# Kernel optimization log

Measured on AMD Instinct MI355X. Metric: run time of the kernel, lower is better.

Reference implementation:

```python
import jax, jax.numpy as jnp
import numpy as np

N = 100000      # nodes
D = 128         # input feature dim
K = 8           # propagation hops (concat K+1 blocks)
HID = 512
OUT = 32
E = 1600000     # edges (avg degree 16)
BN_EPS = 1e-5
DEG_EPS = 1e-8


def setup_inputs() -> dict:
    key = jax.random.key(0)
    ks = jax.random.split(key, 8)
    feature = jax.random.normal(ks[0], (N, D), dtype=jnp.float32)
    coor = jax.random.uniform(ks[1], (N, 2), dtype=jnp.float32)
    edge_index = jax.random.randint(ks[2], (2, E), 0, N, dtype=jnp.int32)
    theta = jnp.array(1.0, dtype=jnp.float32)  # Gaussian bandwidth param
    fan1 = D * (K + 1)
    W1 = jax.random.normal(ks[3], (HID, fan1), dtype=jnp.float32) * (1.0 / np.sqrt(fan1))
    b1 = jnp.zeros((HID,), dtype=jnp.float32)
    gamma = jnp.ones((HID,), dtype=jnp.float32)
    beta = jnp.zeros((HID,), dtype=jnp.float32)
    W2 = jax.random.normal(ks[4], (OUT, HID), dtype=jnp.float32) * (1.0 / np.sqrt(HID))
    b2 = jnp.zeros((OUT,), dtype=jnp.float32)
    return {"feature": feature, "coor": coor, "theta": theta,
            "W1": W1, "b1": b1, "gamma": gamma, "beta": beta,
            "W2": W2, "b2": b2, "edge_index": edge_index, "m": 1}


def reference(feature, coor, theta, W1, b1, gamma, beta, W2, b2, edge_index, m):
    row, col = edge_index[0], edge_index[1]  # dst, src
    # Gaussian kernel edge weights from coordinate distances (gather on coor)
    diff = coor[row] - coor[col]                       # [E, 2]
    dist2 = jnp.sum(diff * diff, axis=-1)              # [E]
    w = jnp.exp(-dist2 * theta / m)                    # [E]
    # degree (row) normalization via scatter-add
    deg = jax.ops.segment_sum(w, row, num_segments=N)  # [N]
    norm = w / (deg[row] + DEG_EPS)                    # [E]
    # K sequential propagations, concat with input (-> N x D*(K+1))
    xs = [feature]
    x = feature
    for _ in range(K):
        msgs = x[col] * norm[:, None]                  # [E, D] gather + weight
        x = jax.ops.segment_sum(msgs, row, num_segments=N)  # [N, D] scatter
        xs.append(x)
    h = jnp.concatenate(xs, axis=-1)                   # [N, D*(K+1)]
    # MLP head: fc1 -> leaky_relu(0.2) -> BatchNorm1d (batch stats) -> fc2
    h = jax.nn.leaky_relu(h @ W1.T + b1, negative_slope=0.2)
    mu = jnp.mean(h, axis=0)
    var = jnp.var(h, axis=0)
    h = (h - mu) * jax.lax.rsqrt(var + BN_EPS) * gamma + beta
    # dropout omitted (deterministic/eval reference)
    return h @ W2.T + b2
```

## Files before the change

### kernel.cpp

```cpp
#include <hip/hip_runtime.h>
#include <hip/hip_bf16.h>
#include <cstdint>
#include <cstddef>

#define NNODES 100000
#define DFEAT 128
#define KHOP 8
#define FAN1 1152
#define HIDN 512
#define OUTD 32
#define NEDGE 1600000
#define BN_EPS 1e-5f
#define DEG_EPS 1e-8f

using short8 = __attribute__((ext_vector_type(8))) short;
using f32x4  = __attribute__((ext_vector_type(4))) float;

__device__ __forceinline__ float bf16lo(uint32_t u) { return __uint_as_float(u << 16); }
__device__ __forceinline__ float bf16hi(uint32_t u) { return __uint_as_float(u & 0xffff0000u); }
__device__ __forceinline__ float bf16s(short x) {
    return __uint_as_float(((uint32_t)(uint16_t)x) << 16);
}
__device__ __forceinline__ uint32_t packbf(float a, float b) {
    uint32_t lo = __bfloat16_as_ushort(__float2bfloat16(a));
    uint32_t hi = __bfloat16_as_ushort(__float2bfloat16(b));
    return lo | (hi << 16);
}

__device__ __forceinline__ void gload16(const void* g, void* l) {
    __builtin_amdgcn_global_load_lds(
        (const __attribute__((address_space(1))) uint32_t*)g,
        (__attribute__((address_space(3))) uint32_t*)l, 16, 0, 0);
}

struct Blk9 { const __hip_bfloat16* p[9]; };

__global__ __launch_bounds__(256) void edge_kernel(
    const int* __restrict__ ei, const float* __restrict__ coor,
    const float* __restrict__ theta, const int* __restrict__ mm,
    float* __restrict__ deg, int* __restrict__ cnt)
{
    int e = blockIdx.x * 256 + threadIdx.x;
    if (e >= NEDGE) return;
    float tom = theta[0] / (float)mm[0];
    int r = ei[e], c = ei[NEDGE + e];
    float2 pr = *(const float2*)(coor + 2*(size_t)r);
    float2 pc = *(const float2*)(coor + 2*(size_t)c);
    float dx = pr.x - pc.x, dy = pr.y - pc.y;
    float w = expf(-(dx*dx + dy*dy) * tom);
    atomicAdd(&deg[r], w);
    atomicAdd(&cnt[r], 1);
}

__global__ __launch_bounds__(1024) void scan_local(
    const int* __restrict__ cnt, int* __restrict__ row_ptr,
    int* __restrict__ bsum, int n)
{
    __shared__ int wsum[16];
    int b = blockIdx.x, tid = threadIdx.x;
    int i = b * 1024 + tid;
    int lane = tid & 63, wv = tid >> 6;
    int v = (i < n) ? cnt[i] : 0;
    #pragma unroll
    for (int off = 1; off < 64; off <<= 1) {
        int t = __shfl_up(v, off, 64);
        if (lane >= off) v += t;
    }
    if (lane == 63) wsum[wv] = v;
    __syncthreads();
    if (tid < 16) {
        int t = wsum[tid];
        #pragma unroll
        for (int off = 1; off < 16; off <<= 1) {
            int u = __shfl_up(t, off, 64);
            if (tid >= off) t += u;
        }
        wsum[tid] = t;
    }
    __syncthreads();
    int incl = v + ((wv == 0) ? 0 : wsum[wv - 1]);
    if (i < n) row_ptr[i + 1] = incl;
    if (tid == 0) bsum[b] = wsum[15];
}

__global__ __launch_bounds__(128) void scan_carry(int* __restrict__ bsum, int n)
{
    __shared__ int ws[2];
    int tid = threadIdx.x, lane = tid & 63, wv = tid >> 6;
    int v = (tid < n) ? bsum[tid] : 0;
    int incl = v;
    #pragma unroll
    for (int off = 1; off < 64; off <<= 1) {
        int t = __shfl_up(incl, off, 64);
        if (lane >= off) incl += t;
    }
    if (lane == 63) ws[wv] = incl;
    __syncthreads();
    int excl = incl - v + ((wv == 0) ? 0 : ws[0]);
    if (tid < n) bsum[tid] = excl;
}

__global__ __launch_bounds__(256) void scan_add(
    const int* __restrict__ bsum, int* __restrict__ row_ptr, int n)
{
    int i = blockIdx.x * 256 + threadIdx.x;
    if (i == 0) row_ptr[0] = 0;
    if (i < n) row_ptr[i + 1] += bsum[i >> 10];
}

__global__ __launch_bounds__(256) void fill_kernel(
    const int* __restrict__ ei, const float* __restrict__ coor,
    const float* __restrict__ theta, const int* __restrict__ mm,
    const float* __restrict__ deg, const int* __restrict__ row_ptr,
    int* __restrict__ fill, int* __restrict__ cols, float* __restrict__ nrm)
{
    int e = blockIdx.x * 256 + threadIdx.x;
    if (e >= NEDGE) return;
    float tom = theta[0] / (float)mm[0];
    int r = ei[e], c = ei[NEDGE + e];
    float2 pr = *(const float2*)(coor + 2*(size_t)r);
    float2 pc = *(const float2*)(coor + 2*(size_t)c);
    float dx = pr.x - pc.x, dy = pr.y - pc.y;
    float w = expf(-(dx*dx + dy*dy) * tom);
    int pos = row_ptr[r] + atomicAdd(&fill[r], 1);
    cols[pos] = c;
    nrm[pos] = w / (deg[r] + DEG_EPS);
}

__global__ __launch_bounds__(256) void cast_feat_kernel(
    const float* __restrict__ f, __hip_bfloat16* __restrict__ x0)
{
    int i = blockIdx.x * 256 + threadIdx.x;
    int node = i >> 6, l2 = i & 63;
    if (node >= NNODES) return;
    float2 v = *(const float2*)(f + (size_t)node * DFEAT + l2 * 2);
    __hip_bfloat162 hb;
    hb.x = __float2bfloat16(v.x);
    hb.y = __float2bfloat16(v.y);
    *(__hip_bfloat162*)(x0 + (size_t)node * DFEAT + l2 * 2) = hb;
}

__global__ __launch_bounds__(256) void cast_w1_kernel(
    const float* __restrict__ w1, __hip_bfloat16* __restrict__ o)
{
    int i = blockIdx.x * 256 + threadIdx.x;
    if (i < HIDN * FAN1) o[i] = __float2bfloat16(w1[i]);
}

__global__ __launch_bounds__(256) void prop_kernel(
    const __hip_bfloat16* __restrict__ x, __hip_bfloat16* __restrict__ y,
    const int* __restrict__ row_ptr, const int* __restrict__ cols,
    const float* __restrict__ nrm)
{
    int gw = (blockIdx.x * 256 + threadIdx.x) >> 6;
    if (gw >= NNODES) return;
    int lane = threadIdx.x & 63;
    int q = lane >> 4, sl = lane & 15;
    int beg = row_ptr[gw], end = row_ptr[gw + 1];
    float a0 = 0.f, a1 = 0.f, a2 = 0.f, a3 = 0.f;
    float a4 = 0.f, a5 = 0.f, a6 = 0.f, a7 = 0.f;
    int e = beg + q;
    for (; e + 12 < end; e += 16) {
        int s0 = cols[e], s1 = cols[e + 4], s2 = cols[e + 8], s3 = cols[e + 12];
        float w0 = nrm[e], w1 = nrm[e + 4], w2 = nrm[e + 8], w3 = nrm[e + 12];
        uint4 u0 = *(const uint4*)(x + (size_t)s0 * DFEAT + sl * 8);
        uint4 u1 = *(const uint4*)(x + (size_t)s1 * DFEAT + sl * 8);
        uint4 u2 = *(const uint4*)(x + (size_t)s2 * DFEAT + sl * 8);
        uint4 u3 = *(const uint4*)(x + (size_t)s3 * DFEAT + sl * 8);
        a0 += w0 * bf16lo(u0.x); a1 += w0 * bf16hi(u0.x);
        a2 += w0 * bf16lo(u0.y); a3 += w0 * bf16hi(u0.y);
        a4 += w0 * bf16lo(u0.z); a5 += w0 * bf16hi(u0.z);
        a6 += w0 * bf16lo(u0.w); a7 += w0 * bf16hi(u0.w);
        a0 += w1 * bf16lo(u1.x); a1 += w1 * bf16hi(u1.x);
        a2 += w1 * bf16lo(u1.y); a3 += w1 * bf16hi(u1.y);
        a4 += w1 * bf16lo(u1.z); a5 += w1 * bf16hi(u1.z);
        a6 += w1 * bf16lo(u1.w); a7 += w1 * bf16hi(u1.w);
        a0 += w2 * bf16lo(u2.x); a1 += w2 * bf16hi(u2.x);
        a2 += w2 * bf16lo(u2.y); a3 += w2 * bf16hi(u2.y);
        a4 += w2 * bf16lo(u2.z); a5 += w2 * bf16hi(u2.z);
        a6 += w2 * bf16lo(u2.w); a7 += w2 * bf16hi(u2.w);
        a0 += w3 * bf16lo(u3.x); a1 += w3 * bf16hi(u3.x);
        a2 += w3 * bf16lo(u3.y); a3 += w3 * bf16hi(u3.y);
        a4 += w3 * bf16lo(u3.z); a5 += w3 * bf16hi(u3.z);
        a6 += w3 * bf16lo(u3.w); a7 += w3 * bf16hi(u3.w);
    }
    for (; e < end; e += 4) {
        int s0 = cols[e];
        float w0 = nrm[e];
        uint4 u0 = *(const uint4*)(x + (size_t)s0 * DFEAT + sl * 8);
        a0 += w0 * bf16lo(u0.x); a1 += w0 * bf16hi(u0.x);
        a2 += w0 * bf16lo(u0.y); a3 += w0 * bf16hi(u0.y);
        a4 += w0 * bf16lo(u0.z); a5 += w0 * bf16hi(u0.z);
        a6 += w0 * bf16lo(u0.w); a7 += w0 * bf16hi(u0.w);
    }
    a0 += __shfl_xor(a0, 16, 64); a0 += __shfl_xor(a0, 32, 64);
    a1 += __shfl_xor(a1, 16, 64); a1 += __shfl_xor(a1, 32, 64);
    a2 += __shfl_xor(a2, 16, 64); a2 += __shfl_xor(a2, 32, 64);
    a3 += __shfl_xor(a3, 16, 64); a3 += __shfl_xor(a3, 32, 64);
    a4 += __shfl_xor(a4, 16, 64); a4 += __shfl_xor(a4, 32, 64);
    a5 += __shfl_xor(a5, 16, 64); a5 += __shfl_xor(a5, 32, 64);
    a6 += __shfl_xor(a6, 16, 64); a6 += __shfl_xor(a6, 32, 64);
    a7 += __shfl_xor(a7, 16, 64); a7 += __shfl_xor(a7, 32, 64);
    if (q == 0) {
        uint4 o;
        o.x = packbf(a0, a1);
        o.y = packbf(a2, a3);
        o.z = packbf(a4, a5);
        o.w = packbf(a6, a7);
        *(uint4*)(y + (size_t)gw * DFEAT + sl * 8) = o;
    }
}

__global__ __launch_bounds__(256) void fc1_kernel(
    Blk9 blks, const __hip_bfloat16* __restrict__ w1,
    const float* __restrict__ b1, __hip_bfloat16* __restrict__ h1,
    float* __restrict__ gsum, float* __restrict__ gsq,
    int nblk, int kb0, int mode)
{
    __shared__ char smem[33792];
    int pid = blockIdx.x;
    int lid = (pid & 7) * 391 + (pid >> 3);
    int n0 = (lid & 3) * 128;
    int m0 = (lid >> 2) * 128;
    int tid = threadIdx.x, lane = tid & 63, wv = tid >> 6;
    int wr = wv >> 1, wc = wv & 1;

    f32x4 acc[4][4];
    #pragma unroll
    for (int i = 0; i < 4; ++i)
        #pragma unroll
        for (int j = 0; j < 4; ++j)
            acc[i][j] = (f32x4){0.f, 0.f, 0.f, 0.f};

    int nkt = nblk * 4;

#define STAGE(hb, ktv) do {                                                   \
        const __hip_bfloat16* xp = blks.p[(ktv) >> 2];                        \
        int koff_ = ((ktv) & 3) * 32;                                         \
        int kglob_ = (kb0 + ((ktv) >> 2)) * 128 + koff_;                      \
        char* Ab_ = smem + (hb) * 16384;                                      \
        char* Bb_ = Ab_ + 8192;                                               \
        _Pragma("unroll")                                                     \
        for (int l = 0; l < 2; ++l) {                                         \
            int u = l * 256 + wv * 64 + lane;                                 \
            int row_ = u >> 2, qq_ = u & 3;                                   \
            gload16(xp + (size_t)(m0 + row_) * DFEAT + koff_ + qq_ * 8,       \
                    Ab_ + u * 16);                                            \
            gload16(w1 + (size_t)(n0 + row_) * FAN1 + kglob_ + qq_ * 8,       \
                    Bb_ + u * 16);                                            \
        }                                                                     \
    } while (0)

    STAGE(0, 0);
    for (int kt = 0; kt < nkt; ++kt) {
        int cur = kt & 1;
        __builtin_amdgcn_s_barrier();
        if (kt + 1 < nkt) {
            STAGE(cur ^ 1, kt + 1);
            asm volatile("s_waitcnt vmcnt(4)" ::: "memory");
        } else {
            asm volatile("s_waitcnt vmcnt(0)" ::: "memory");
        }
        __builtin_amdgcn_s_barrier();
        char* Ab = smem + cur * 16384;
        char* Bb = Ab + 8192;
        short8 af[4], bfr[4];
        #pragma unroll
        for (int i = 0; i < 4; ++i)
            af[i] = *(const short8*)(Ab + (wr * 64 + i * 16 + (lane & 15)) * 64 + (lane >> 4) * 16);
        #pragma unroll
        for (int j = 0; j < 4; ++j)
            bfr[j] = *(const short8*)(Bb + (wc * 64 + j * 16 + (lane & 15)) * 64 + (lane >> 4) * 16);
        #pragma unroll
        for (int j = 0; j < 4; ++j)
            #pragma unroll
            for (int i = 0; i < 4; ++i)
                acc[i][j] = __builtin_amdgcn_mfma_f32_16x16x32_bf16(af[i], bfr[j], acc[i][j], 0, 0, 0);
    }
#undef STAGE

    __syncthreads();
    __hip_bfloat16* tile = (__hip_bfloat16*)smem;
    float* lsum = (float*)(smem + 32768);
    float* lsq  = lsum + 128;
    bool fin = (mode & 2) != 0;
    if (fin && tid < 128) { lsum[tid] = 0.f; lsq[tid] = 0.f; }
    #pragma unroll
    for (int i = 0; i < 4; ++i) {
        #pragma unroll
        for (int j = 0; j < 4; ++j) {
            int col = wc * 64 + j * 16 + (lane & 15);
            #pragma unroll
            for (int r = 0; r < 4; ++r) {
                int row = wr * 64 + i * 16 + (lane >> 4) * 4 + r;
                tile[row * 128 + col] = __float2bfloat16(acc[i][j][r]);
            }
        }
    }
    __syncthreads();

    int cu = tid & 15, tr = tid >> 4;
    float bias[8];
    float s[8], q[8];
    #pragma unroll
    for (int e = 0; e < 8; ++e) { s[e] = 0.f; q[e] = 0.f; }
    if (fin) {
        #pragma unroll
        for (int e = 0; e < 8; ++e) bias[e] = b1[n0 + cu * 8 + e];
    }
    for (int p = 0; p < 8; ++p) {
        int row = p * 16 + tr;
        int gm = m0 + row;
        if (gm >= NNODES) continue;
        short8 fresh = *(const short8*)(tile + row * 128 + cu * 8);
        size_t gidx = (size_t)gm * HIDN + n0 + cu * 8;
        float v[8];
        #pragma unroll
        for (int e = 0; e < 8; ++e) v[e] = bf16s(fresh[e]);
        if (mode & 1) {
            short8 prev = *(const short8*)(h1 + gidx);
            #pragma unroll
            for (int e = 0; e < 8; ++e) v[e] += bf16s(prev[e]);
        }
        if (fin) {
            #pragma unroll
            for (int e = 0; e < 8; ++e) {
                float t = v[e] + bias[e];
                t = (t > 0.f) ? t : 0.2f * t;
                v[e] = t;
                s[e] += t;
                q[e] += t * t;
            }
        }
        short8 outv;
        #pragma unroll
        for (int e = 0; e < 8; ++e) outv[e] = (short)__bfloat16_as_ushort(__float2bfloat16(v[e]));
        *(short8*)(h1 + gidx) = outv;
    }
    if (fin) {
        #pragma unroll
        for (int e = 0; e < 8; ++e) {
            atomicAdd(&lsum[cu * 8 + e], s[e]);
            atomicAdd(&lsq[cu * 8 + e], q[e]);
        }
        __syncthreads();
        if (tid < 128) {
            atomicAdd(&gsum[n0 + tid], lsum[tid]);
            atomicAdd(&gsq[n0 + tid], lsq[tid]);
        }
    }
}

__global__ __launch_bounds__(512) void bn_finalize(
    const float* __restrict__ gsum, const float* __restrict__ gsq,
    const float* __restrict__ gamma, const float* __restrict__ beta,
    const float* __restrict__ w2, const float* __restrict__ b2,
    __hip_bfloat16* __restrict__ w2s, float* __restrict__ cvec)
{
    __shared__ float ts[HIDN];
    int tid = threadIdx.x;
    float mu = gsum[tid] * (1.0f / NNODES);
    float var = gsq[tid] * (1.0f / NNODES) - mu * mu;
    float s = gamma[tid] * rsqrtf(var + BN_EPS);
    float t = beta[tid] - mu * s;
    ts[tid] = t;
    for (int o = 0; o < OUTD; ++o)
        w2s[o * HIDN + tid] = __float2bfloat16(w2[o * HIDN + tid] * s);
    __syncthreads();
    int lane = tid & 63, wv = tid >> 6;
    for (int o = wv; o < OUTD; o += 8) {
        float p = 0.f;
        for (int j = lane; j < HIDN; j += 64) p += ts[j] * w2[o * HIDN + j];
        #pragma unroll
        for (int off = 32; off; off >>= 1) p += __shfl_xor(p, off, 64);
        if (lane == 0) cvec[o] = p + b2[o];
    }
}

__global__ __launch_bounds__(256) void fc2_kernel(
    const __hip_bfloat16* __restrict__ h1, const __hip_bfloat16* __restrict__ w2s,
    const float* __restrict__ cvec, float* __restrict__ out)
{
    int gw = (blockIdx.x * 256 + threadIdx.x) >> 6;
    if (gw >= NNODES / 16) return;
    int lane = threadIdx.x & 63;
    int m0 = gw * 16;
    f32x4 acc[2];
    acc[0] = (f32x4){0.f, 0.f, 0.f, 0.f};
    acc[1] = (f32x4){0.f, 0.f, 0.f, 0.f};
    #pragma unroll
    for (int kt = 0; kt < HIDN / 32; ++kt) {
        int k0 = kt * 32;
        short8 a = *(const short8*)(h1 + (size_t)(m0 + (lane & 15)) * HIDN + k0 + (lane >> 4) * 8);
        #pragma unroll
        for (int j = 0; j < 2; ++j) {
            short8 b = *(const short8*)(w2s + (size_t)(j * 16 + (lane & 15)) * HIDN + k0 + (lane >> 4) * 8);
            acc[j] = __builtin_amdgcn_mfma_f32_16x16x32_bf16(a, b, acc[j], 0, 0, 0);
        }
    }
    #pragma unroll
    for (int j = 0; j < 2; ++j) {
        int col = j * 16 + (lane & 15);
        float cadd = cvec[col];
        #pragma unroll
        for (int r = 0; r < 4; ++r) {
            int row = m0 + (lane >> 4) * 4 + r;
            out[(size_t)row * OUTD + col] = acc[j][r] + cadd;
        }
    }
}

struct Ptrs {
    float *deg, *nrm, *gsum, *gsq, *cvec;
    int *cnt, *fillc, *row_ptr, *colsb, *bsum;
    __hip_bfloat16 *slot[9], *h1acc, *w1b, *w2s;
};

static size_t layout(char* base, int nslots, Ptrs& P) {
    char* p = base;
    auto take = [&](size_t b) {
        char* q = (char*)(((uintptr_t)p + 255) & ~(uintptr_t)255);
        p = q + b;
        return q;
    };
    P.deg     = (float*)take((size_t)NNODES * 4);
    P.cnt     = (int*)  take((size_t)NNODES * 4);
    P.fillc   = (int*)  take((size_t)NNODES * 4);
    P.row_ptr = (int*)  take((size_t)(NNODES + 1) * 4);
    P.bsum    = (int*)  take(128 * 4);
    P.colsb   = (int*)  take((size_t)NEDGE * 4);
    P.nrm     = (float*)take((size_t)NEDGE * 4);
    P.h1acc   = (__hip_bfloat16*)take((size_t)NNODES * HIDN * 2);
    P.w1b     = (__hip_bfloat16*)take((size_t)HIDN * FAN1 * 2);
    P.w2s     = (__hip_bfloat16*)take((size_t)OUTD * HIDN * 2);
    P.gsum    = (float*)take(HIDN * 4);
    P.gsq     = (float*)take(HIDN * 4);
    P.cvec    = (float*)take(OUTD * 4);
    for (int i = 0; i < 9; ++i) P.slot[i] = nullptr;
    for (int i = 0; i < nslots; ++i)
        P.slot[i] = (__hip_bfloat16*)take((size_t)NNODES * DFEAT * 2 + 32768);
    return (size_t)(p - base);
}

extern "C" void kernel_launch(void* const* d_in, const int* in_sizes, int n_in,
                              void* d_out, int out_size, void* d_ws, size_t ws_size,
                              hipStream_t stream)
{
    const float* feature = (const float*)d_in[0];
    const float* coor    = (const float*)d_in[1];
    const float* theta   = (const float*)d_in[2];
    const float* W1      = (const float*)d_in[3];
    const float* b1      = (const float*)d_in[4];
    const float* gamma   = (const float*)d_in[5];
    const float* beta    = (const float*)d_in[6];
    const float* W2      = (const float*)d_in[7];
    const float* b2      = (const float*)d_in[8];
    const int*   ei      = (const int*)d_in[9];
    const int*   mm      = (const int*)d_in[10];
    float* out = (float*)d_out;
    (void)in_sizes; (void)n_in; (void)out_size;

    Ptrs P;
    size_t need9 = layout((char*)0, 9, P);
    size_t need5 = layout((char*)0, 5, P);
    int nslots = (ws_size >= need9) ? 9 : (ws_size >= need5) ? 5 : 3;
    layout((char*)d_ws, nslots, P);

    hipMemsetAsync(P.deg,   0, (size_t)NNODES * 4, stream);
    hipMemsetAsync(P.cnt,   0, (size_t)NNODES * 4, stream);
    hipMemsetAsync(P.fillc, 0, (size_t)NNODES * 4, stream);
    hipMemsetAsync(P.gsum,  0, HIDN * 4, stream);
    hipMemsetAsync(P.gsq,   0, HIDN * 4, stream);

    int eb = (NEDGE + 255) / 256;
    int nchunk = (NNODES + 1023) / 1024;
    edge_kernel<<<eb, 256, 0, stream>>>(ei, coor, theta, mm, P.deg, P.cnt);
    scan_local<<<nchunk, 1024, 0, stream>>>(P.cnt, P.row_ptr, P.bsum, NNODES);
    scan_carry<<<1, 128, 0, stream>>>(P.bsum, nchunk);
    scan_add<<<(NNODES + 255) / 256, 256, 0, stream>>>(P.bsum, P.row_ptr, NNODES);
    fill_kernel<<<eb, 256, 0, stream>>>(ei, coor, theta, mm, P.deg, P.row_ptr,
                                        P.fillc, P.colsb, P.nrm);

    cast_w1_kernel<<<(HIDN * FAN1 + 255) / 256, 256, 0, stream>>>(W1, P.w1b);
    cast_feat_kernel<<<(NNODES * 64) / 256, 256, 0, stream>>>(feature, P.slot[0]);

    int pb = (NNODES * 64) / 256;
    int fgrid = 8 * 391;

    auto launch_fc1 = [&](int first_slot, int nblk, int kb0, int mode) {
        Blk9 b;
        for (int i = 0; i < 9; ++i) b.p[i] = P.slot[0];
        for (int i = 0; i < nblk; ++i) b.p[i] = P.slot[(first_slot + i) % nslots];
        fc1_kernel<<<fgrid, 256, 0, stream>>>(b, P.w1b, b1, P.h1acc,
                                              P.gsum, P.gsq, nblk, kb0, mode);
    };

    for (int k = 1; k <= KHOP; ++k) {
        prop_kernel<<<pb, 256, 0, stream>>>(P.slot[(k - 1) % nslots],
                                            P.slot[k % nslots],
                                            P.row_ptr, P.colsb, P.nrm);
        if (nslots == 5 && k == 4) launch_fc1(0, 5, 0, 0);
        if (nslots == 3 && k == 2) launch_fc1(0, 3, 0, 0);
        if (nslots == 3 && k == 5) launch_fc1(0, 3, 3, 1);
    }
    if (nslots == 9) launch_fc1(0, 9, 0, 2);
    if (nslots == 5) launch_fc1(0, 4, 5, 3);
    if (nslots == 3) launch_fc1(0, 3, 6, 3);

    bn_finalize<<<1, 512, 0, stream>>>(P.gsum, P.gsq, gamma, beta, W2, b2,
                                       P.w2s, P.cvec);
    fc2_kernel<<<(NNODES / 16 * 64 + 255) / 256, 256, 0, stream>>>(P.h1acc, P.w2s,
                                                                   P.cvec, out);
}
```

Measured before the change: 1.012 ms.

## Always use 3-slot rolling fc1 with 128x64 tiles and scheduling barriers

```diff
diff --git a/kernel.cpp b/kernel.cpp
--- a/kernel.cpp
+++ b/kernel.cpp
@@ -33,7 +33,7 @@
         (__attribute__((address_space(3))) uint32_t*)l, 16, 0, 0);
 }
 
-struct Blk9 { const __hip_bfloat16* p[9]; };
+struct Blk3 { const __hip_bfloat16* p[3]; };
 
 __global__ __launch_bounds__(256) void edge_kernel(
     const int* __restrict__ ei, const float* __restrict__ coor,
@@ -212,33 +212,30 @@
 }
 
 __global__ __launch_bounds__(256) void fc1_kernel(
-    Blk9 blks, const __hip_bfloat16* __restrict__ w1,
+    Blk3 blks, const __hip_bfloat16* __restrict__ w1,
     const float* __restrict__ b1, __hip_bfloat16* __restrict__ h1,
     float* __restrict__ gsum, float* __restrict__ gsq,
-    int nblk, int kb0, int mode)
-{
-    __shared__ char smem[33792];
+    int nkt, int kb0, int mode)
+{
+    __shared__ char smem[25088];
     int pid = blockIdx.x;
-    int lid = (pid & 7) * 391 + (pid >> 3);
-    int n0 = (lid & 3) * 128;
-    int m0 = (lid >> 2) * 128;
+    int t = (pid & 7) * 782 + (pid >> 3);
+    int m0 = (t >> 3) * 128, n0 = (t & 7) * 64;
     int tid = threadIdx.x, lane = tid & 63, wv = tid >> 6;
     int wr = wv >> 1, wc = wv & 1;
 
-    f32x4 acc[4][4];
+    f32x4 acc[4][2];
     #pragma unroll
     for (int i = 0; i < 4; ++i)
         #pragma unroll
-        for (int j = 0; j < 4; ++j)
+        for (int j = 0; j < 2; ++j)
             acc[i][j] = (f32x4){0.f, 0.f, 0.f, 0.f};
-
-    int nkt = nblk * 4;
 
 #define STAGE(hb, ktv) do {                                                   \
         const __hip_bfloat16* xp = blks.p[(ktv) >> 2];                        \
         int koff_ = ((ktv) & 3) * 32;                                         \
         int kglob_ = (kb0 + ((ktv) >> 2)) * 128 + koff_;                      \
-        char* Ab_ = smem + (hb) * 16384;                                      \
+        char* Ab_ = smem + (hb) * 12288;                                      \
         char* Bb_ = Ab_ + 8192;                                               \
         _Pragma("unroll")                                                     \
         for (int l = 0; l < 2; ++l) {                                         \
@@ -246,6 +243,10 @@
             int row_ = u >> 2, qq_ = u & 3;                                   \
             gload16(xp + (size_t)(m0 + row_) * DFEAT + koff_ + qq_ * 8,       \
                     Ab_ + u * 16);                                            \
+        }                                                                     \
+        {                                                                     \
+            int u = wv * 64 + lane;                                           \
+            int row_ = u >> 2, qq_ = u & 3;                                   \
             gload16(w1 + (size_t)(n0 + row_) * FAN1 + kglob_ + qq_ * 8,       \
                     Bb_ + u * 16);                                            \
         }                                                                     \
@@ -254,25 +255,28 @@
     STAGE(0, 0);
     for (int kt = 0; kt < nkt; ++kt) {
         int cur = kt & 1;
+        __builtin_amdgcn_sched_barrier(0);
         __builtin_amdgcn_s_barrier();
+        __builtin_amdgcn_sched_barrier(0);
         if (kt + 1 < nkt) {
             STAGE(cur ^ 1, kt + 1);
-            asm volatile("s_waitcnt vmcnt(4)" ::: "memory");
+            asm volatile("s_waitcnt vmcnt(3)" ::: "memory");
         } else {
             asm volatile("s_waitcnt vmcnt(0)" ::: "memory");
         }
         __builtin_amdgcn_s_barrier();
-        char* Ab = smem + cur * 16384;
+        __builtin_amdgcn_sched_barrier(0);
+        char* Ab = smem + cur * 12288;
         char* Bb = Ab + 8192;
-        short8 af[4], bfr[4];
+        short8 af[4], bfr[2];
         #pragma unroll
         for (int i = 0; i < 4; ++i)
             af[i] = *(const short8*)(Ab + (wr * 64 + i * 16 + (lane & 15)) * 64 + (lane >> 4) * 16);
         #pragma unroll
-        for (int j = 0; j < 4; ++j)
-            bfr[j] = *(const short8*)(Bb + (wc * 64 + j * 16 + (lane & 15)) * 64 + (lane >> 4) * 16);
-        #pragma unroll
-        for (int j = 0; j < 4; ++j)
+        for (int j = 0; j < 2; ++j)
+            bfr[j] = *(const short8*)(Bb + (wc * 32 + j * 16 + (lane & 15)) * 64 + (lane >> 4) * 16);
+        #pragma unroll
+        for (int j = 0; j < 2; ++j)
             #pragma unroll
             for (int i = 0; i < 4; ++i)
                 acc[i][j] = __builtin_amdgcn_mfma_f32_16x16x32_bf16(af[i], bfr[j], acc[i][j], 0, 0, 0);
@@ -281,25 +285,25 @@
 
     __syncthreads();
     __hip_bfloat16* tile = (__hip_bfloat16*)smem;
-    float* lsum = (float*)(smem + 32768);
-    float* lsq  = lsum + 128;
+    float* lsum = (float*)(smem + 24576);
+    float* lsq  = lsum + 64;
     bool fin = (mode & 2) != 0;
-    if (fin && tid < 128) { lsum[tid] = 0.f; lsq[tid] = 0.f; }
+    if (fin && tid < 64) { lsum[tid] = 0.f; lsq[tid] = 0.f; }
     #pragma unroll
     for (int i = 0; i < 4; ++i) {
         #pragma unroll
-        for (int j = 0; j < 4; ++j) {
-            int col = wc * 64 + j * 16 + (lane & 15);
+        for (int j = 0; j < 2; ++j) {
+            int col = wc * 32 + j * 16 + (lane & 15);
             #pragma unroll
             for (int r = 0; r < 4; ++r) {
                 int row = wr * 64 + i * 16 + (lane >> 4) * 4 + r;
-                tile[row * 128 + col] = __float2bfloat16(acc[i][j][r]);
+                tile[row * 64 + col] = __float2bfloat16(acc[i][j][r]);
             }
         }
     }
     __syncthreads();
 
-    int cu = tid & 15, tr = tid >> 4;
+    int cu = tid & 7, tr = tid >> 3;
     float bias[8];
     float s[8], q[8];
     #pragma unroll
@@ -308,11 +312,12 @@
         #pragma unroll
         for (int e = 0; e < 8; ++e) bias[e] = b1[n0 + cu * 8 + e];
     }
-    for (int p = 0; p < 8; ++p) {
-        int row = p * 16 + tr;
+    #pragma unroll
+    for (int p = 0; p < 4; ++p) {
+        int row = p * 32 + tr;
         int gm = m0 + row;
         if (gm >= NNODES) continue;
-        short8 fresh = *(const short8*)(tile + row * 128 + cu * 8);
+        short8 fresh = *(const short8*)(tile + row * 64 + cu * 8);
         size_t gidx = (size_t)gm * HIDN + n0 + cu * 8;
         float v[8];
         #pragma unroll
@@ -325,11 +330,11 @@
         if (fin) {
             #pragma unroll
             for (int e = 0; e < 8; ++e) {
-                float t = v[e] + bias[e];
-                t = (t > 0.f) ? t : 0.2f * t;
-                v[e] = t;
-                s[e] += t;
-                q[e] += t * t;
+                float tv = v[e] + bias[e];
+                tv = (tv > 0.f) ? tv : 0.2f * tv;
+                v[e] = tv;
+                s[e] += tv;
+                q[e] += tv * tv;
             }
         }
         short8 outv;
@@ -344,7 +349,7 @@
             atomicAdd(&lsq[cu * 8 + e], q[e]);
         }
         __syncthreads();
-        if (tid < 128) {
+        if (tid < 64) {
             atomicAdd(&gsum[n0 + tid], lsum[tid]);
             atomicAdd(&gsq[n0 + tid], lsq[tid]);
         }
@@ -413,10 +418,10 @@
 struct Ptrs {
     float *deg, *nrm, *gsum, *gsq, *cvec;
     int *cnt, *fillc, *row_ptr, *colsb, *bsum;
-    __hip_bfloat16 *slot[9], *h1acc, *w1b, *w2s;
+    __hip_bfloat16 *slot[3], *h1acc, *w1b, *w2s;
 };
 
-static size_t layout(char* base, int nslots, Ptrs& P) {
+static size_t layout(char* base, Ptrs& P) {
     char* p = base;
     auto take = [&](size_t b) {
         char* q = (char*)(((uintptr_t)p + 255) & ~(uintptr_t)255);
@@ -436,9 +441,8 @@
     P.gsum    = (float*)take(HIDN * 4);
     P.gsq     = (float*)take(HIDN * 4);
     P.cvec    = (float*)take(OUTD * 4);
-    for (int i = 0; i < 9; ++i) P.slot[i] = nullptr;
-    for (int i = 0; i < nslots; ++i)
-        P.slot[i] = (__hip_bfloat16*)take((size_t)NNODES * DFEAT * 2 + 32768);
+    for (int i = 0; i < 3; ++i)
+        P.slot[i] = (__hip_bfloat16*)take((size_t)NNODES * DFEAT * 2 + 65536);
     return (size_t)(p - base);
 }
 
@@ -458,13 +462,10 @@
     const int*   ei      = (const int*)d_in[9];
     const int*   mm      = (const int*)d_in[10];
     float* out = (float*)d_out;
-    (void)in_sizes; (void)n_in; (void)out_size;
+    (void)in_sizes; (void)n_in; (void)out_size; (void)ws_size;
 
     Ptrs P;
-    size_t need9 = layout((char*)0, 9, P);
-    size_t need5 = layout((char*)0, 5, P);
-    int nslots = (ws_size >= need9) ? 9 : (ws_size >= need5) ? 5 : 3;
-    layout((char*)d_ws, nslots, P);
+    layout((char*)d_ws, P);
 
     hipMemsetAsync(P.deg,   0, (size_t)NNODES * 4, stream);
     hipMemsetAsync(P.cnt,   0, (size_t)NNODES * 4, stream);
@@ -485,27 +486,23 @@
     cast_feat_kernel<<<(NNODES * 64) / 256, 256, 0, stream>>>(feature, P.slot[0]);
 
     int pb = (NNODES * 64) / 256;
-    int fgrid = 8 * 391;
-
-    auto launch_fc1 = [&](int first_slot, int nblk, int kb0, int mode) {
-        Blk9 b;
-        for (int i = 0; i < 9; ++i) b.p[i] = P.slot[0];
-        for (int i = 0; i < nblk; ++i) b.p[i] = P.slot[(first_slot + i) % nslots];
+    int fgrid = 8 * 782;
+
+    auto launch_fc1 = [&](int kb0, int mode) {
+        Blk3 b;
+        for (int i = 0; i < 3; ++i) b.p[i] = P.slot[i];
         fc1_kernel<<<fgrid, 256, 0, stream>>>(b, P.w1b, b1, P.h1acc,
-                                              P.gsum, P.gsq, nblk, kb0, mode);
+                                              P.gsum, P.gsq, 12, kb0, mode);
     };
 
     for (int k = 1; k <= KHOP; ++k) {
-        prop_kernel<<<pb, 256, 0, stream>>>(P.slot[(k - 1) % nslots],
-                                            P.slot[k % nslots],
+        prop_kernel<<<pb, 256, 0, stream>>>(P.slot[(k - 1) % 3],
+                                            P.slot[k % 3],
                                             P.row_ptr, P.colsb, P.nrm);
-        if (nslots == 5 && k == 4) launch_fc1(0, 5, 0, 0);
-        if (nslots == 3 && k == 2) launch_fc1(0, 3, 0, 0);
-        if (nslots == 3 && k == 5) launch_fc1(0, 3, 3, 1);
-    }
-    if (nslots == 9) launch_fc1(0, 9, 0, 2);
-    if (nslots == 5) launch_fc1(0, 4, 5, 3);
-    if (nslots == 3) launch_fc1(0, 3, 6, 3);
+        if (k == 2) launch_fc1(0, 0);
+        if (k == 5) launch_fc1(3, 1);
+    }
+    launch_fc1(6, 3);
 
     bn_finalize<<<1, 512, 0, stream>>>(P.gsum, P.gsq, gamma, beta, W2, b2,
                                        P.w2s, P.cvec);
```

Measured after the change: 1.110 ms. 9.7% more time.

## Always use three feature slots and block h1 layout by 128-column panels

Applied to the files above, without the earlier changes.

```diff
diff --git a/kernel.cpp b/kernel.cpp
--- a/kernel.cpp
+++ b/kernel.cpp
@@ -33,7 +33,7 @@
         (__attribute__((address_space(3))) uint32_t*)l, 16, 0, 0);
 }
 
-struct Blk9 { const __hip_bfloat16* p[9]; };
+struct Blk3 { const __hip_bfloat16* p[3]; };
 
 __global__ __launch_bounds__(256) void edge_kernel(
     const int* __restrict__ ei, const float* __restrict__ coor,
@@ -212,10 +212,10 @@
 }
 
 __global__ __launch_bounds__(256) void fc1_kernel(
-    Blk9 blks, const __hip_bfloat16* __restrict__ w1,
-    const float* __restrict__ b1, __hip_bfloat16* __restrict__ h1,
+    Blk3 blks, const __hip_bfloat16* __restrict__ w1,
+    const float* __restrict__ b1, __hip_bfloat16* __restrict__ h1b,
     float* __restrict__ gsum, float* __restrict__ gsq,
-    int nblk, int kb0, int mode)
+    int nkt, int kb0, int mode)
 {
     __shared__ char smem[33792];
     int pid = blockIdx.x;
@@ -231,8 +231,6 @@
         #pragma unroll
         for (int j = 0; j < 4; ++j)
             acc[i][j] = (f32x4){0.f, 0.f, 0.f, 0.f};
-
-    int nkt = nblk * 4;
 
 #define STAGE(hb, ktv) do {                                                   \
         const __hip_bfloat16* xp = blks.p[(ktv) >> 2];                        \
@@ -308,17 +306,18 @@
         #pragma unroll
         for (int e = 0; e < 8; ++e) bias[e] = b1[n0 + cu * 8 + e];
     }
+    size_t blkbase = (size_t)(n0 >> 7) * NNODES * 128;
     for (int p = 0; p < 8; ++p) {
         int row = p * 16 + tr;
         int gm = m0 + row;
         if (gm >= NNODES) continue;
         short8 fresh = *(const short8*)(tile + row * 128 + cu * 8);
-        size_t gidx = (size_t)gm * HIDN + n0 + cu * 8;
+        size_t gidx = blkbase + (size_t)gm * 128 + cu * 8;
         float v[8];
         #pragma unroll
         for (int e = 0; e < 8; ++e) v[e] = bf16s(fresh[e]);
         if (mode & 1) {
-            short8 prev = *(const short8*)(h1 + gidx);
+            short8 prev = *(const short8*)(h1b + gidx);
             #pragma unroll
             for (int e = 0; e < 8; ++e) v[e] += bf16s(prev[e]);
         }
@@ -335,7 +334,7 @@
         short8 outv;
         #pragma unroll
         for (int e = 0; e < 8; ++e) outv[e] = (short)__bfloat16_as_ushort(__float2bfloat16(v[e]));
-        *(short8*)(h1 + gidx) = outv;
+        *(short8*)(h1b + gidx) = outv;
     }
     if (fin) {
         #pragma unroll
@@ -378,7 +377,7 @@
 }
 
 __global__ __launch_bounds__(256) void fc2_kernel(
-    const __hip_bfloat16* __restrict__ h1, const __hip_bfloat16* __restrict__ w2s,
+    const __hip_bfloat16* __restrict__ h1b, const __hip_bfloat16* __restrict__ w2s,
     const float* __restrict__ cvec, float* __restrict__ out)
 {
     int gw = (blockIdx.x * 256 + threadIdx.x) >> 6;
@@ -391,7 +390,9 @@
     #pragma unroll
     for (int kt = 0; kt < HIDN / 32; ++kt) {
         int k0 = kt * 32;
-        short8 a = *(const short8*)(h1 + (size_t)(m0 + (lane & 15)) * HIDN + k0 + (lane >> 4) * 8);
+        short8 a = *(const short8*)(h1b
+            + ((size_t)(kt >> 2) * NNODES + (m0 + (lane & 15))) * 128
+            + (kt & 3) * 32 + (lane >> 4) * 8);
         #pragma unroll
         for (int j = 0; j < 2; ++j) {
             short8 b = *(const short8*)(w2s + (size_t)(j * 16 + (lane & 15)) * HIDN + k0 + (lane >> 4) * 8);
@@ -413,10 +414,10 @@
 struct Ptrs {
     float *deg, *nrm, *gsum, *gsq, *cvec;
     int *cnt, *fillc, *row_ptr, *colsb, *bsum;
-    __hip_bfloat16 *slot[9], *h1acc, *w1b, *w2s;
+    __hip_bfloat16 *slot[3], *h1acc, *w1b, *w2s;
 };
 
-static size_t layout(char* base, int nslots, Ptrs& P) {
+static size_t layout(char* base, Ptrs& P) {
     char* p = base;
     auto take = [&](size_t b) {
         char* q = (char*)(((uintptr_t)p + 255) & ~(uintptr_t)255);
@@ -430,14 +431,13 @@
     P.bsum    = (int*)  take(128 * 4);
     P.colsb   = (int*)  take((size_t)NEDGE * 4);
     P.nrm     = (float*)take((size_t)NEDGE * 4);
-    P.h1acc   = (__hip_bfloat16*)take((size_t)NNODES * HIDN * 2);
+    P.h1acc   = (__hip_bfloat16*)take((size_t)NNODES * HIDN * 2 + 65536);
     P.w1b     = (__hip_bfloat16*)take((size_t)HIDN * FAN1 * 2);
     P.w2s     = (__hip_bfloat16*)take((size_t)OUTD * HIDN * 2);
     P.gsum    = (float*)take(HIDN * 4);
     P.gsq     = (float*)take(HIDN * 4);
     P.cvec    = (float*)take(OUTD * 4);
-    for (int i = 0; i < 9; ++i) P.slot[i] = nullptr;
-    for (int i = 0; i < nslots; ++i)
+    for (int i = 0; i < 3; ++i)
         P.slot[i] = (__hip_bfloat16*)take((size_t)NNODES * DFEAT * 2 + 32768);
     return (size_t)(p - base);
 }
@@ -458,13 +458,10 @@
     const int*   ei      = (const int*)d_in[9];
     const int*   mm      = (const int*)d_in[10];
     float* out = (float*)d_out;
-    (void)in_sizes; (void)n_in; (void)out_size;
+    (void)in_sizes; (void)n_in; (void)out_size; (void)ws_size;
 
     Ptrs P;
-    size_t need9 = layout((char*)0, 9, P);
-    size_t need5 = layout((char*)0, 5, P);
-    int nslots = (ws_size >= need9) ? 9 : (ws_size >= need5) ? 5 : 3;
-    layout((char*)d_ws, nslots, P);
+    layout((char*)d_ws, P);
 
     hipMemsetAsync(P.deg,   0, (size_t)NNODES * 4, stream);
     hipMemsetAsync(P.cnt,   0, (size_t)NNODES * 4, stream);
@@ -487,25 +484,21 @@
     int pb = (NNODES * 64) / 256;
     int fgrid = 8 * 391;
 
-    auto launch_fc1 = [&](int first_slot, int nblk, int kb0, int mode) {
-        Blk9 b;
-        for (int i = 0; i < 9; ++i) b.p[i] = P.slot[0];
-        for (int i = 0; i < nblk; ++i) b.p[i] = P.slot[(first_slot + i) % nslots];
+    auto launch_fc1 = [&](int kb0, int mode) {
+        Blk3 b;
+        for (int i = 0; i < 3; ++i) b.p[i] = P.slot[i];
         fc1_kernel<<<fgrid, 256, 0, stream>>>(b, P.w1b, b1, P.h1acc,
-                                              P.gsum, P.gsq, nblk, kb0, mode);
+                                              P.gsum, P.gsq, 12, kb0, mode);
     };
 
     for (int k = 1; k <= KHOP; ++k) {
-        prop_kernel<<<pb, 256, 0, stream>>>(P.slot[(k - 1) % nslots],
-                                            P.slot[k % nslots],
+        prop_kernel<<<pb, 256, 0, stream>>>(P.slot[(k - 1) % 3],
+                                            P.slot[k % 3],
                                             P.row_ptr, P.colsb, P.nrm);
-        if (nslots == 5 && k == 4) launch_fc1(0, 5, 0, 0);
-        if (nslots == 3 && k == 2) launch_fc1(0, 3, 0, 0);
-        if (nslots == 3 && k == 5) launch_fc1(0, 3, 3, 1);
-    }
-    if (nslots == 9) launch_fc1(0, 9, 0, 2);
-    if (nslots == 5) launch_fc1(0, 4, 5, 3);
-    if (nslots == 3) launch_fc1(0, 3, 6, 3);
+        if (k == 2) launch_fc1(0, 0);
+        if (k == 5) launch_fc1(3, 1);
+    }
+    launch_fc1(6, 3);
 
     bn_finalize<<<1, 512, 0, stream>>>(P.gsum, P.gsq, gamma, beta, W2, b2,
                                        P.w2s, P.cvec);
```

Measured after the change: 1.030 ms. About the same (+1.8%).
